# Kernel optimization log

Measured on AMD Instinct MI355X. Metric: run time of the kernel, lower is better.

## Reference

```python
import jax, jax.numpy as jnp
import numpy as np

D_MODEL = 1024
NHEAD = 16
D_HEAD = D_MODEL // NHEAD
DIM_FF = 4096
EPS = 1e-5

def layer_norm(x, scale, bias):
    mu = jnp.mean(x, axis=-1, keepdims=True)
    var = jnp.mean(jnp.square(x - mu), axis=-1, keepdims=True)
    return (x - mu) * jax.lax.rsqrt(var + EPS) * scale + bias

def setup_inputs() -> dict:
    key = jax.random.key(0)
    ks = jax.random.split(key, 8)
    B, T, D = 4, 2048, D_MODEL
    s = 1.0 / np.sqrt(D)
    sf = 1.0 / np.sqrt(DIM_FF)
    return {
        "x": jax.random.normal(ks[0], (B, T, D), dtype=jnp.float32),
        "ln1_scale": jnp.ones((D,), jnp.float32),
        "ln1_bias": jnp.zeros((D,), jnp.float32),
        "qkv_w": jax.random.normal(ks[1], (3 * D, D), jnp.float32) * s,  # torch Linear weight [out,in]
        "out_w": jax.random.normal(ks[2], (D, D), jnp.float32) * s,
        "ln2_scale": jnp.ones((D,), jnp.float32),
        "ln2_bias": jnp.zeros((D,), jnp.float32),
        "fc1_w": jax.random.normal(ks[3], (DIM_FF, D), jnp.float32) * s,
        "fc1_b": jnp.zeros((DIM_FF,), jnp.float32),
        "fc2_w": jax.random.normal(ks[4], (D, DIM_FF), jnp.float32) * sf,
        "fc2_b": jnp.zeros((D,), jnp.float32),
    }

def reference(x, ln1_scale, ln1_bias, qkv_w, out_w, ln2_scale, ln2_bias, fc1_w, fc1_b, fc2_w, fc2_b):
    B, T, D = x.shape
    # --- attention sublayer (pre-LN) ---
    h = layer_norm(x, ln1_scale, ln1_bias)
    qkv = jnp.einsum('btd,ed->bte', h, qkv_w)  # [B,T,3D]
    q, k, v = jnp.split(qkv, 3, axis=-1)
    def heads(t):
        return t.reshape(B, T, NHEAD, D_HEAD).transpose(0, 2, 1, 3)  # [B,H,T,dh]
    q, k, v = heads(q), heads(k), heads(v)
    scores = jnp.einsum('bhqd,bhkd->bhqk', q, k) / np.sqrt(D_HEAD)
    attn = jax.nn.softmax(scores, axis=-1)
    o = jnp.einsum('bhqk,bhkd->bhqd', attn, v)
    o = o.transpose(0, 2, 1, 3).reshape(B, T, D)
    h = jnp.einsum('btd,ed->bte', o, out_w)
    x = x + h
    # --- FFN sublayer (pre-LN) ---
    h = layer_norm(x, ln2_scale, ln2_bias)
    h = jnp.einsum('btd,fd->btf', h, fc1_w) + fc1_b
    h = jax.nn.gelu(h, approximate=False)
    h = jnp.einsum('btf,df->btd', h, fc2_w) + fc2_b
    return x + h
```

## Files before the change

### kernel.cpp

```cpp
#include <hip/hip_runtime.h>
#include <hip/hip_bf16.h>
#include <math.h>

typedef unsigned short u16;
typedef unsigned int u32;
typedef short s8v __attribute__((ext_vector_type(8)));
typedef float f4v __attribute__((ext_vector_type(4)));
typedef float f16v __attribute__((ext_vector_type(16)));
typedef u32 u4v __attribute__((ext_vector_type(4)));

#define D_MODEL 1024
#define DIMFF   4096
#define SEQ     2048
#define TOKENS  8192

#define QSCALE 0.18033688011112042f

static __device__ __forceinline__ u16 f2bf(float f) {
    unsigned int u = __builtin_bit_cast(unsigned int, f);
    unsigned int lsb = (u >> 16) & 1u;
    u += 0x7fffu + lsb;
    return (u16)(u >> 16);
}

static __device__ __forceinline__ float gelu_fast(float z) {
    float z2 = z * z;
    float p  = fmaf(z2, -0.1029472255f, -2.3021867892f);
    float e  = __builtin_amdgcn_exp2f(z * p);
    return z * __builtin_amdgcn_rcpf(1.0f + e);
}

static __device__ __forceinline__ void gl2lds16(const u16* g, u16* l) {
    __builtin_amdgcn_global_load_lds(
        (__attribute__((address_space(1))) void*)(void*)g,
        (__attribute__((address_space(3))) void*)l, 16, 0, 0);
}

#define N4_QKV  786432
#define N4_WO   262144
#define N4_FC   1048576
__global__ __launch_bounds__(256) void cvt_all_kernel(const float* __restrict__ s0,
                                                      const float* __restrict__ s1,
                                                      const float* __restrict__ s2,
                                                      const float* __restrict__ s3,
                                                      u16* __restrict__ dst) {
    int i = blockIdx.x * 256 + threadIdx.x;
    const float* src; int j;
    if (i < N4_QKV)                    { src = s0; j = i; }
    else if (i < N4_QKV + N4_WO)       { src = s1; j = i - N4_QKV; }
    else if (i < N4_QKV + N4_WO + N4_FC) { src = s2; j = i - N4_QKV - N4_WO; }
    else                               { src = s3; j = i - N4_QKV - N4_WO - N4_FC; }
    float4 v = ((const float4*)src)[j];
    ushort4 o;
    o.x = f2bf(v.x); o.y = f2bf(v.y); o.z = f2bf(v.z); o.w = f2bf(v.w);
    ((ushort4*)dst)[i] = o;
}

__global__ __launch_bounds__(256) void ln_kernel(const float* __restrict__ x,
                                                 const float* __restrict__ scale,
                                                 const float* __restrict__ bias,
                                                 u16* __restrict__ out) {
    int row = blockIdx.x;
    int t = threadIdx.x;
    const float* xr = x + (size_t)row * D_MODEL;
    float4 v = ((const float4*)xr)[t];
    float s  = v.x + v.y + v.z + v.w;
    float ss = v.x*v.x + v.y*v.y + v.z*v.z + v.w*v.w;
    #pragma unroll
    for (int off = 1; off < 64; off <<= 1) {
        s  += __shfl_xor(s, off);
        ss += __shfl_xor(ss, off);
    }
    __shared__ float red[8];
    int wave = t >> 6, lane = t & 63;
    if (lane == 0) { red[wave] = s; red[4 + wave] = ss; }
    __syncthreads();
    float S  = red[0] + red[1] + red[2] + red[3];
    float SS = red[4] + red[5] + red[6] + red[7];
    float mu  = S * (1.0f / D_MODEL);
    float var = SS * (1.0f / D_MODEL) - mu * mu;
    float r = rsqrtf(var + 1e-5f);
    float4 sc = ((const float4*)scale)[t];
    float4 bi = ((const float4*)bias)[t];
    ushort4 o;
    o.x = f2bf((v.x - mu) * r * sc.x + bi.x);
    o.y = f2bf((v.y - mu) * r * sc.y + bi.y);
    o.z = f2bf((v.z - mu) * r * sc.z + bi.z);
    o.w = f2bf((v.w - mu) * r * sc.w + bi.w);
    ((ushort4*)(out + (size_t)row * D_MODEL))[t] = o;
}

#define BM 128
#define BN 128
#define BK 64

template<int MODE>
__global__ __launch_bounds__(256) void gemm_kernel(
        const u16* __restrict__ A, const u16* __restrict__ W,
        const float* __restrict__ bias, const float* __restrict__ res,
        void* __restrict__ outp, void* __restrict__ out2, int M, int N, int K) {
    __shared__ __attribute__((aligned(16))) u16 As[BM * BK];
    __shared__ __attribute__((aligned(16))) u16 Bs[BN * BK];
    int t = threadIdx.x;
    int lane = t & 63, w = t >> 6;
    int nb = N / BN;
    int bm = blockIdx.x / nb, bn = blockIdx.x % nb;
    int m0 = bm * BM, n0 = bn * BN;
    int wm = (w >> 1) * 64, wn = (w & 1) * 64;
    int lr = lane >> 4, lc = lane & 15, sw = lc & 7;

    f4v acc[4][4] = {};

    int arow[4], acg[4];
    #pragma unroll
    for (int n = 0; n < 4; ++n) {
        int chunk = (w * 4 + n) * 64 + lane;
        arow[n] = chunk >> 3;
        acg[n]  = ((chunk & 7) ^ (arow[n] & 7)) * 8;
    }

    for (int k0 = 0; k0 < K; k0 += BK) {
        #pragma unroll
        for (int n = 0; n < 4; ++n) {
            gl2lds16(&A[(size_t)(m0 + arow[n]) * K + k0 + acg[n]], &As[(w * 4 + n) * 512]);
            gl2lds16(&W[(size_t)(n0 + arow[n]) * K + k0 + acg[n]], &Bs[(w * 4 + n) * 512]);
        }
        __syncthreads();
        #pragma unroll
        for (int ks = 0; ks < 2; ++ks) {
            s8v af[4], bfr[4];
            #pragma unroll
            for (int i = 0; i < 4; ++i)
                af[i] = *(const s8v*)&As[(wm + i * 16 + lc) * BK + ((ks * 4 + lr) ^ sw) * 8];
            #pragma unroll
            for (int j = 0; j < 4; ++j)
                bfr[j] = *(const s8v*)&Bs[(wn + j * 16 + lc) * BK + ((ks * 4 + lr) ^ sw) * 8];
            #pragma unroll
            for (int i = 0; i < 4; ++i)
                #pragma unroll
                for (int j = 0; j < 4; ++j) {
                    if (MODE == 4)
                        acc[i][j] = __builtin_amdgcn_mfma_f32_16x16x32_bf16(af[i], bfr[j], acc[i][j], 0, 0, 0);
                    else
                        acc[i][j] = __builtin_amdgcn_mfma_f32_16x16x32_bf16(bfr[j], af[i], acc[i][j], 0, 0, 0);
                }
        }
        __syncthreads();
    }

    if (MODE == 4) {
        #pragma unroll
        for (int i = 0; i < 4; ++i) {
            #pragma unroll
            for (int j = 0; j < 4; ++j) {
                int col = n0 + wn + j * 16 + lc;
                int colbase = n0 + wn + j * 16;
                if (colbase < 2048) {
                    float sc = (colbase < 1024) ? QSCALE : 1.0f;
                    #pragma unroll
                    for (int r = 0; r < 4; ++r) {
                        int row = m0 + wm + i * 16 + lr * 4 + r;
                        ((u16*)outp)[(size_t)row * 2048 + col] = f2bf(acc[i][j][r] * sc);
                    }
                } else {
                    int dlin = col - 2048;
                    int h = dlin >> 6, dd = dlin & 63;
                    int trow = m0 + wm + i * 16 + lr * 4;
                    int bb = trow >> 11, tt = trow & 2047;
                    int bh = bb * 16 + h;
                    ushort4 vv;
                    vv.x = f2bf(acc[i][j][0]); vv.y = f2bf(acc[i][j][1]);
                    vv.z = f2bf(acc[i][j][2]); vv.w = f2bf(acc[i][j][3]);
                    *(ushort4*)&((u16*)out2)[((size_t)bh * 64 + dd) * SEQ + tt] = vv;
                }
            }
        }
    } else {
        #pragma unroll
        for (int j = 0; j < 4; ++j) {
            int colb = n0 + wn + j * 16 + lr * 4;
            float4 b4;
            if (MODE != 1) b4 = *(const float4*)&bias[colb];
            #pragma unroll
            for (int i = 0; i < 4; ++i) {
                int row = m0 + wm + i * 16 + lc;
                size_t idx = (size_t)row * N + colb;
                f4v a = acc[i][j];
                if (MODE == 2) {
                    ushort4 o;
                    o.x = f2bf(gelu_fast(a[0] + b4.x));
                    o.y = f2bf(gelu_fast(a[1] + b4.y));
                    o.z = f2bf(gelu_fast(a[2] + b4.z));
                    o.w = f2bf(gelu_fast(a[3] + b4.w));
                    *(ushort4*)&((u16*)outp)[idx] = o;
                } else {
                    float4 rr = *(const float4*)&res[idx];
                    float4 o;
                    if (MODE == 3) {
                        o.x = rr.x + a[0] + b4.x; o.y = rr.y + a[1] + b4.y;
                        o.z = rr.z + a[2] + b4.z; o.w = rr.w + a[3] + b4.w;
                    } else {
                        o.x = rr.x + a[0]; o.y = rr.y + a[1];
                        o.z = rr.z + a[2]; o.w = rr.w + a[3];
                    }
                    *(float4*)&((float*)outp)[idx] = o;
                }
            }
        }
    }
}

__global__ __launch_bounds__(256) void attn_kernel(const u16* __restrict__ qk,
                                                   const u16* __restrict__ vt,
                                                   u16* __restrict__ out) {
    __shared__ __attribute__((aligned(16))) u16 Ks[64 * 64];
    __shared__ __attribute__((aligned(16))) u16 Vts[64 * 64];
    __shared__ __attribute__((aligned(16))) u16 Ps[128 * 68];
    __shared__ float l_s[128];
    int t = threadIdx.x, lane = t & 63, w = t >> 6;
    int l31 = lane & 31, hi = lane >> 5;
    int blk = blockIdx.x;
    int bh = blk & 63, qt = blk >> 6;
    int b = bh >> 4, h = bh & 15;
    size_t tok0 = (size_t)b * SEQ;
    int q0 = qt * 128;

    s8v bq[4];
    {
        const u16* qp = qk + (tok0 + q0 + w * 32 + l31) * 2048 + h * 64 + hi * 8;
        #pragma unroll
        for (int dch = 0; dch < 4; ++dch) bq[dch] = *(const s8v*)(qp + dch * 16);
    }
    f16v o[2] = {};
    float lp = 0.f;

    int srow[2], scg[2];
    #pragma unroll
    for (int n = 0; n < 2; ++n) {
        int chunk = (w * 2 + n) * 64 + lane;
        srow[n] = chunk >> 3;
        scg[n]  = ((chunk & 7) ^ (srow[n] & 7)) * 8;
    }
    const u16* vbase = vt + (size_t)bh * 64 * SEQ;
    int prow = (w * 32 + l31) * 68;

    for (int kt = 0; kt < SEQ / 64; ++kt) {
        #pragma unroll
        for (int n = 0; n < 2; ++n) {
            gl2lds16(&qk[(tok0 + kt * 64 + srow[n]) * 2048 + 1024 + h * 64 + scg[n]],
                     &Ks[(w * 2 + n) * 512]);
            gl2lds16(&vbase[(size_t)srow[n] * SEQ + kt * 64 + scg[n]],
                     &Vts[(w * 2 + n) * 512]);
        }
        __syncthreads();

        f16v s_[2] = {};
        #pragma unroll
        for (int kb = 0; kb < 2; ++kb)
            #pragma unroll
            for (int dch = 0; dch < 4; ++dch) {
                s8v ak = *(const s8v*)&Ks[(kb * 32 + l31) * 64 + ((dch * 2 + hi) ^ (l31 & 7)) * 8];
                s_[kb] = __builtin_amdgcn_mfma_f32_32x32x16_bf16(ak, bq[dch], s_[kb], 0, 0, 0);
            }

        #pragma unroll
        for (int kb = 0; kb < 2; ++kb)
            #pragma unroll
            for (int g = 0; g < 4; ++g) {
                u32 ib[4];
                #pragma unroll
                for (int rr = 0; rr < 4; ++rr) {
                    ib[rr] = (u32)fmaf(s_[kb][g * 4 + rr], 8388608.0f, 1064992506.0f);
                    lp += __builtin_bit_cast(float, ib[rr]);
                }
                uint2 pk;
                pk.x = __builtin_amdgcn_perm(ib[1], ib[0], 0x07060302);
                pk.y = __builtin_amdgcn_perm(ib[3], ib[2], 0x07060302);
                *(uint2*)&Ps[prow + kb * 32 + g * 8 + hi * 4] = pk;
            }

        #pragma unroll
        for (int ch = 0; ch < 4; ++ch) {
            uint2 u0 = *(const uint2*)&Ps[prow + ch * 16 + hi * 8];
            uint2 u1 = *(const uint2*)&Ps[prow + ch * 16 + hi * 8 + 4];
            u4v tmp; tmp.x = u0.x; tmp.y = u0.y; tmp.z = u1.x; tmp.w = u1.y;
            s8v ap = __builtin_bit_cast(s8v, tmp);
            #pragma unroll
            for (int dblk = 0; dblk < 2; ++dblk) {
                s8v bv = *(const s8v*)&Vts[(dblk * 32 + l31) * 64 + ((ch * 2 + hi) ^ (l31 & 7)) * 8];
                o[dblk] = __builtin_amdgcn_mfma_f32_32x32x16_bf16(ap, bv, o[dblk], 0, 0, 0);
            }
        }
        __syncthreads();
    }

    lp += __shfl_xor(lp, 32);
    l_s[w * 32 + l31] = 1.0f / lp;
    #pragma unroll
    for (int r = 0; r < 16; ++r) {
        int qrl = (r & 3) + 8 * (r >> 2) + 4 * hi;
        float linv = l_s[w * 32 + qrl];
        size_t row = tok0 + q0 + w * 32 + qrl;
        #pragma unroll
        for (int dblk = 0; dblk < 2; ++dblk)
            out[row * 1024 + h * 64 + dblk * 32 + l31] = f2bf(o[dblk][r] * linv);
    }
}

extern "C" void kernel_launch(void* const* d_in, const int* in_sizes, int n_in,
                              void* d_out, int out_size, void* d_ws, size_t ws_size,
                              hipStream_t stream) {
    const float* x      = (const float*)d_in[0];
    const float* ln1_s  = (const float*)d_in[1];
    const float* ln1_b  = (const float*)d_in[2];
    const float* qkv_w  = (const float*)d_in[3];
    const float* out_w  = (const float*)d_in[4];
    const float* ln2_s  = (const float*)d_in[5];
    const float* ln2_b  = (const float*)d_in[6];
    const float* fc1_w  = (const float*)d_in[7];
    const float* fc1_b  = (const float*)d_in[8];
    const float* fc2_w  = (const float*)d_in[9];
    const float* fc2_b  = (const float*)d_in[10];
    float* out = (float*)d_out;

    char* ws = (char*)d_ws;
    size_t off = 0;
    auto alloc = [&](size_t bytes) -> void* {
        void* p = ws + off;
        off += (bytes + 255) & ~(size_t)255;
        return p;
    };
    u16* wq  = (u16*)alloc((size_t)3072 * 1024 * 2);
    u16* wo  = (u16*)alloc((size_t)1024 * 1024 * 2);
    u16* w1  = (u16*)alloc((size_t)4096 * 1024 * 2);
    u16* w2  = (u16*)alloc((size_t)1024 * 4096 * 2);
    u16* h1  = (u16*)alloc((size_t)TOKENS * 1024 * 2);
    u16* qk  = (u16*)alloc((size_t)TOKENS * 2048 * 2);
    float* x2 = (float*)alloc((size_t)TOKENS * 1024 * 4);
    u16* g   = (u16*)alloc((size_t)TOKENS * 4096 * 2);
    u16* attn_out = h1;
    u16* h2       = qk;
    u16* vt       = (u16*)x2;
    (void)wo; (void)w1; (void)w2;

    cvt_all_kernel<<<(N4_QKV + N4_WO + 2 * N4_FC) / 256, 256, 0, stream>>>(
        qkv_w, out_w, fc1_w, fc2_w, wq);

    ln_kernel<<<TOKENS, 256, 0, stream>>>(x, ln1_s, ln1_b, h1);
    gemm_kernel<4><<<(TOKENS / BM) * (3072 / BN), 256, 0, stream>>>(
        h1, wq, nullptr, nullptr, qk, vt, TOKENS, 3072, 1024);
    attn_kernel<<<64 * 16, 256, 0, stream>>>(qk, vt, attn_out);
    gemm_kernel<1><<<(TOKENS / BM) * (1024 / BN), 256, 0, stream>>>(
        attn_out, wo, nullptr, x, x2, nullptr, TOKENS, 1024, 1024);
    ln_kernel<<<TOKENS, 256, 0, stream>>>(x2, ln2_s, ln2_b, h2);
    gemm_kernel<2><<<(TOKENS / BM) * (DIMFF / BN), 256, 0, stream>>>(
        h2, w1, fc1_b, nullptr, g, nullptr, TOKENS, DIMFF, 1024);
    gemm_kernel<3><<<(TOKENS / BM) * (1024 / BN), 256, 0, stream>>>(
        g, w2, fc2_b, x2, out, nullptr, TOKENS, 1024, DIMFF);
}
```

Baseline: 515.0 us.

## Rewrite GEMM as multi-stage pipelined 256-row tiles with 512-thread blocks

Replaces the single-buffered 128x128x64 GEMM with a 256xBN tile over BK=32, using a 4- or 6-deep LDS ring fed by global_load_lds. Loads are issued several stages ahead and waited on with explicit vmcnt counts, raw s_barrier and sched_barrier, and MFMA bursts get raised wave priority. Wide GEMMs split the B tile into two phases. The aim is to hide global-load latency behind MFMA work and raise per-wave reuse. In exchange it needs more registers and LDS, and the hand-tuned waitcnt logic is fragile.

```diff
diff --git a/kernel.cpp b/kernel.cpp
--- a/kernel.cpp
+++ b/kernel.cpp
@@ -34,6 +34,20 @@
     __builtin_amdgcn_global_load_lds(
         (__attribute__((address_space(1))) void*)(void*)g,
         (__attribute__((address_space(3))) void*)l, 16, 0, 0);
+}
+
+static __device__ __forceinline__ void bar() {
+    __builtin_amdgcn_sched_barrier(0);
+    asm volatile("" ::: "memory");
+    __builtin_amdgcn_s_barrier();
+    asm volatile("" ::: "memory");
+    __builtin_amdgcn_sched_barrier(0);
+}
+
+template<int N> static __device__ __forceinline__ void vwait() {
+    if constexpr (N == 8)       asm volatile("s_waitcnt vmcnt(8)" ::: "memory");
+    else if constexpr (N == 12) asm volatile("s_waitcnt vmcnt(12)" ::: "memory");
+    else                        asm volatile("s_waitcnt vmcnt(0)" ::: "memory");
 }
 
 #define N4_QKV  786432
@@ -90,69 +104,131 @@
     ((ushort4*)(out + (size_t)row * D_MODEL))[t] = o;
 }
 
-#define BM 128
-#define BN 128
-#define BK 64
-
-template<int MODE>
-__global__ __launch_bounds__(256) void gemm_kernel(
+template<int MODE, int BN_, int NPH, int DEPTH>
+__global__ __launch_bounds__(512, 2) void gemm_kernel(
         const u16* __restrict__ A, const u16* __restrict__ W,
         const float* __restrict__ bias, const float* __restrict__ res,
         void* __restrict__ outp, void* __restrict__ out2, int M, int N, int K) {
-    __shared__ __attribute__((aligned(16))) u16 As[BM * BK];
-    __shared__ __attribute__((aligned(16))) u16 Bs[BN * BK];
+    constexpr int BM = 256, BK = 32;
+    constexpr int NFN = BN_ / 64;
+    constexpr int RA = 2;
+    constexpr int RB = BN_ / 128;
+    constexpr int S = DEPTH - 1;
+    constexpr int VST = (RA + RB) * (S - 1);
+    constexpr int ASZ = BM * BK, BSZ = BN_ * BK;
+    __shared__ __attribute__((aligned(16))) u16 As[DEPTH * ASZ];
+    __shared__ __attribute__((aligned(16))) u16 Bs[DEPTH * BSZ];
+
     int t = threadIdx.x;
     int lane = t & 63, w = t >> 6;
-    int nb = N / BN;
+    int lc = lane & 15, lr = lane >> 4;
+    int nb = N / BN_;
     int bm = blockIdx.x / nb, bn = blockIdx.x % nb;
-    int m0 = bm * BM, n0 = bn * BN;
-    int wm = (w >> 1) * 64, wn = (w & 1) * 64;
-    int lr = lane >> 4, lc = lane & 15, sw = lc & 7;
-
-    f4v acc[4][4] = {};
-
-    int arow[4], acg[4];
+    int m0 = bm * BM, n0 = bn * BN_;
+    int wm = (w >> 2) * 128;
+    int wn = (w & 3) * (BN_ / 4);
+    int cxor = (lr ^ (lc & 3)) * 8;
+
+    const u16* Abase = A + (size_t)m0 * K;
+    const u16* Bbase = W + (size_t)n0 * K;
+
+    size_t aoff[RA]; int aldo[RA];
     #pragma unroll
-    for (int n = 0; n < 4; ++n) {
-        int chunk = (w * 4 + n) * 64 + lane;
-        arow[n] = chunk >> 3;
-        acg[n]  = ((chunk & 7) ^ (arow[n] & 7)) * 8;
-    }
-
-    for (int k0 = 0; k0 < K; k0 += BK) {
-        #pragma unroll
-        for (int n = 0; n < 4; ++n) {
-            gl2lds16(&A[(size_t)(m0 + arow[n]) * K + k0 + acg[n]], &As[(w * 4 + n) * 512]);
-            gl2lds16(&W[(size_t)(n0 + arow[n]) * K + k0 + acg[n]], &Bs[(w * 4 + n) * 512]);
-        }
-        __syncthreads();
-        #pragma unroll
-        for (int ks = 0; ks < 2; ++ks) {
-            s8v af[4], bfr[4];
-            #pragma unroll
-            for (int i = 0; i < 4; ++i)
-                af[i] = *(const s8v*)&As[(wm + i * 16 + lc) * BK + ((ks * 4 + lr) ^ sw) * 8];
-            #pragma unroll
-            for (int j = 0; j < 4; ++j)
-                bfr[j] = *(const s8v*)&Bs[(wn + j * 16 + lc) * BK + ((ks * 4 + lr) ^ sw) * 8];
-            #pragma unroll
-            for (int i = 0; i < 4; ++i)
-                #pragma unroll
-                for (int j = 0; j < 4; ++j) {
-                    if (MODE == 4)
-                        acc[i][j] = __builtin_amdgcn_mfma_f32_16x16x32_bf16(af[i], bfr[j], acc[i][j], 0, 0, 0);
-                    else
-                        acc[i][j] = __builtin_amdgcn_mfma_f32_16x16x32_bf16(bfr[j], af[i], acc[i][j], 0, 0, 0);
+    for (int n = 0; n < RA; ++n) {
+        int q = (n * 8 + w) * 64 + lane;
+        int row = q >> 2;
+        aoff[n] = (size_t)row * K + ((q & 3) ^ (row & 3)) * 8;
+        aldo[n] = (n * 8 + w) * 512;
+    }
+    size_t boff[RB]; int bldo[RB];
+    #pragma unroll
+    for (int n = 0; n < RB; ++n) {
+        int q = (n * 8 + w) * 64 + lane;
+        int row = q >> 2;
+        boff[n] = (size_t)row * K + ((q & 3) ^ (row & 3)) * 8;
+        bldo[n] = (n * 8 + w) * 512;
+    }
+
+    const int NT = K / BK;
+    for (int u = 0; u < S; ++u) {
+        size_t kk = (size_t)u * BK;
+        #pragma unroll
+        for (int n = 0; n < RA; ++n) gl2lds16(Abase + aoff[n] + kk, &As[u * ASZ + aldo[n]]);
+        #pragma unroll
+        for (int n = 0; n < RB; ++n) gl2lds16(Bbase + boff[n] + kk, &Bs[u * BSZ + bldo[n]]);
+    }
+    vwait<VST>();
+    bar();
+
+    f4v acc[8][NFN] = {};
+    int cur = 0, sb = S % DEPTH;
+
+    for (int kt = 0; kt < NT; ++kt) {
+        const u16* Ab = &As[cur * ASZ];
+        const u16* Bb = &Bs[cur * BSZ];
+        u16* Asb = &As[sb * ASZ];
+        u16* Bsb = &Bs[sb * BSZ];
+        int kts = kt + S; if (kts >= NT) kts = NT - 1;
+        size_t kk = (size_t)kts * BK;
+
+        s8v af[8];
+        #pragma unroll
+        for (int i = 0; i < 8; ++i)
+            af[i] = *(const s8v*)&Ab[(wm + i * 16 + lc) * BK + cxor];
+        s8v b0 = *(const s8v*)&Bb[(wn + lc) * BK + cxor];
+        s8v b1 = *(const s8v*)&Bb[(wn + 16 + lc) * BK + cxor];
+        #pragma unroll
+        for (int n = 0; n < RA; ++n) gl2lds16(Abase + aoff[n] + kk, Asb + aldo[n]);
+        if constexpr (NPH == 1) {
+            #pragma unroll
+            for (int n = 0; n < RB; ++n) gl2lds16(Bbase + boff[n] + kk, Bsb + bldo[n]);
+        }
+        bar();
+        __builtin_amdgcn_s_setprio(1);
+        #pragma unroll
+        for (int i = 0; i < 8; ++i) {
+            if constexpr (MODE == 4) {
+                acc[i][0] = __builtin_amdgcn_mfma_f32_16x16x32_bf16(af[i], b0, acc[i][0], 0, 0, 0);
+                acc[i][1] = __builtin_amdgcn_mfma_f32_16x16x32_bf16(af[i], b1, acc[i][1], 0, 0, 0);
+            } else {
+                acc[i][0] = __builtin_amdgcn_mfma_f32_16x16x32_bf16(b0, af[i], acc[i][0], 0, 0, 0);
+                acc[i][1] = __builtin_amdgcn_mfma_f32_16x16x32_bf16(b1, af[i], acc[i][1], 0, 0, 0);
+            }
+        }
+        __builtin_amdgcn_s_setprio(0);
+        if constexpr (NPH == 1) vwait<VST>();
+        bar();
+
+        if constexpr (NPH == 2) {
+            s8v b2 = *(const s8v*)&Bb[(wn + 32 + lc) * BK + cxor];
+            s8v b3 = *(const s8v*)&Bb[(wn + 48 + lc) * BK + cxor];
+            #pragma unroll
+            for (int n = 0; n < RB; ++n) gl2lds16(Bbase + boff[n] + kk, Bsb + bldo[n]);
+            bar();
+            __builtin_amdgcn_s_setprio(1);
+            #pragma unroll
+            for (int i = 0; i < 8; ++i) {
+                if constexpr (MODE == 4) {
+                    acc[i][2] = __builtin_amdgcn_mfma_f32_16x16x32_bf16(af[i], b2, acc[i][2], 0, 0, 0);
+                    acc[i][3] = __builtin_amdgcn_mfma_f32_16x16x32_bf16(af[i], b3, acc[i][3], 0, 0, 0);
+                } else {
+                    acc[i][2] = __builtin_amdgcn_mfma_f32_16x16x32_bf16(b2, af[i], acc[i][2], 0, 0, 0);
+                    acc[i][3] = __builtin_amdgcn_mfma_f32_16x16x32_bf16(b3, af[i], acc[i][3], 0, 0, 0);
                 }
-        }
-        __syncthreads();
-    }
-
-    if (MODE == 4) {
-        #pragma unroll
-        for (int i = 0; i < 4; ++i) {
-            #pragma unroll
-            for (int j = 0; j < 4; ++j) {
+            }
+            __builtin_amdgcn_s_setprio(0);
+            vwait<VST>();
+            bar();
+        }
+        cur = (cur + 1 == DEPTH) ? 0 : cur + 1;
+        sb  = (sb + 1 == DEPTH) ? 0 : sb + 1;
+    }
+
+    if constexpr (MODE == 4) {
+        #pragma unroll
+        for (int i = 0; i < 8; ++i) {
+            #pragma unroll
+            for (int j = 0; j < NFN; ++j) {
                 int col = n0 + wn + j * 16 + lc;
                 int colbase = n0 + wn + j * 16;
                 if (colbase < 2048) {
@@ -177,16 +253,16 @@
         }
     } else {
         #pragma unroll
-        for (int j = 0; j < 4; ++j) {
+        for (int j = 0; j < NFN; ++j) {
             int colb = n0 + wn + j * 16 + lr * 4;
             float4 b4;
-            if (MODE != 1) b4 = *(const float4*)&bias[colb];
-            #pragma unroll
-            for (int i = 0; i < 4; ++i) {
+            if constexpr (MODE != 1) b4 = *(const float4*)&bias[colb];
+            #pragma unroll
+            for (int i = 0; i < 8; ++i) {
                 int row = m0 + wm + i * 16 + lc;
                 size_t idx = (size_t)row * N + colb;
                 f4v a = acc[i][j];
-                if (MODE == 2) {
+                if constexpr (MODE == 2) {
                     ushort4 o;
                     o.x = f2bf(gelu_fast(a[0] + b4.x));
                     o.y = f2bf(gelu_fast(a[1] + b4.y));
@@ -196,7 +272,7 @@
                 } else {
                     float4 rr = *(const float4*)&res[idx];
                     float4 o;
-                    if (MODE == 3) {
+                    if constexpr (MODE == 3) {
                         o.x = rr.x + a[0] + b4.x; o.y = rr.y + a[1] + b4.y;
                         o.z = rr.z + a[2] + b4.z; o.w = rr.w + a[3] + b4.w;
                     } else {
@@ -347,14 +423,14 @@
         qkv_w, out_w, fc1_w, fc2_w, wq);
 
     ln_kernel<<<TOKENS, 256, 0, stream>>>(x, ln1_s, ln1_b, h1);
-    gemm_kernel<4><<<(TOKENS / BM) * (3072 / BN), 256, 0, stream>>>(
+    gemm_kernel<4, 256, 2, 4><<<(TOKENS / 256) * (3072 / 256), 512, 0, stream>>>(
         h1, wq, nullptr, nullptr, qk, vt, TOKENS, 3072, 1024);
     attn_kernel<<<64 * 16, 256, 0, stream>>>(qk, vt, attn_out);
-    gemm_kernel<1><<<(TOKENS / BM) * (1024 / BN), 256, 0, stream>>>(
+    gemm_kernel<1, 128, 1, 6><<<(TOKENS / 256) * (1024 / 128), 512, 0, stream>>>(
         attn_out, wo, nullptr, x, x2, nullptr, TOKENS, 1024, 1024);
     ln_kernel<<<TOKENS, 256, 0, stream>>>(x2, ln2_s, ln2_b, h2);
-    gemm_kernel<2><<<(TOKENS / BM) * (DIMFF / BN), 256, 0, stream>>>(
+    gemm_kernel<2, 256, 2, 4><<<(TOKENS / 256) * (DIMFF / 256), 512, 0, stream>>>(
         h2, w1, fc1_b, nullptr, g, nullptr, TOKENS, DIMFF, 1024);
-    gemm_kernel<3><<<(TOKENS / BM) * (1024 / BN), 256, 0, stream>>>(
+    gemm_kernel<3, 128, 1, 6><<<(TOKENS / 256) * (1024 / 128), 512, 0, stream>>>(
         g, w2, fc2_b, x2, out, nullptr, TOKENS, 1024, DIMFF);
 }
```

Result: slower. 542.2 us (+5.3%).
